# Kernel tuning notes

Measured on AMD Instinct MI355X. Metric: run time of the kernel, lower is better.

## Reference

```python
import jax, jax.numpy as jnp
import numpy as np

# Grid config: nuScenes-style BEV grid
XMIN, XMAX, DX = -51.2, 51.2, 0.4
YMIN, YMAX, DY = -51.2, 51.2, 0.4
ZMIN, ZMAX, DZ = -5.0, 3.0, 8.0
NX = int((XMAX - XMIN) / DX)  # 256
NY = int((YMAX - YMIN) / DY)  # 256
NZ = int((ZMAX - ZMIN) / DZ)  # 1
B, N, F = 8, 500000, 18       # batch, points per cloud, radar_feat_dim


def setup_inputs() -> dict:
    key = jax.random.key(0)
    pts = jax.random.normal(key, (B, N, F), dtype=jnp.float32)
    # spread xyz across the [-51.2, 51.2] grid (some points fall outside -> masked)
    pts = pts.at[..., :3].multiply(20.0)
    return {"points": pts}


def reference(points):
    """Scatter-mean rasterization of radar points into a dense BEV grid.

    points: (B, N, 18) float32. Returns (B, F*NZ, NY, NX).
    Equivalent math to the torch running-mean scatter: per-voxel mean of the
    18-dim features of all in-range points falling into that voxel.
    """
    x, y, z = points[..., 0], points[..., 1], points[..., 2]
    mask = ((x >= XMIN) & (x <= XMAX) &
            (y >= YMIN) & (y <= YMAX) &
            (z >= ZMIN) & (z <= ZMAX))
    sx, sy, sz = NX / (XMAX - XMIN), NY / (YMAX - YMIN), NZ / (ZMAX - ZMIN)
    ix = jnp.clip(((x - XMIN) * sx).astype(jnp.int32), 0, NX - 1)
    iy = jnp.clip(((y - YMIN) * sy).astype(jnp.int32), 0, NY - 1)
    iz = jnp.clip(((z - ZMIN) * sz).astype(jnp.int32), 0, NZ - 1)
    # global linear voxel index, batch-offset so one segment_sum covers all B
    lin = (iz * (NY * NX) + iy * NX + ix
           + jnp.arange(B, dtype=jnp.int32)[:, None] * (NZ * NY * NX))
    lin = lin.reshape(-1)                              # (B*N,)
    w = mask.astype(points.dtype).reshape(-1)          # (B*N,) 0/1 weights
    feats = points.reshape(-1, F) * w[:, None]         # masked-out -> 0 contribution
    nseg = B * NZ * NY * NX
    sums = jax.ops.segment_sum(feats, lin, num_segments=nseg)  # (nseg, F)
    cnts = jax.ops.segment_sum(w, lin, num_segments=nseg)      # (nseg,)
    mean = sums / jnp.maximum(cnts, 1.0)[:, None]
    grid = mean.reshape(B, NZ, NY, NX, F)
    grid = jnp.transpose(grid, (0, 4, 1, 2, 3))        # (B, F, NZ, NY, NX)
    return grid.reshape(B, F * NZ, NY, NX)
```

## Files before the change

kernel.cpp:

```cpp
#include <hip/hip_runtime.h>


#define B_     8
#define NPTS   500000
#define F_     18
#define NX_    256
#define NY_    256
#define NVOX   (NX_ * NY_)
#define BN     (B_ * NPTS)
#define NVOXT  (B_ * NVOX)
#define CAP    32

__global__ __launch_bounds__(256) void bin_kernel(const float* __restrict__ pts,
                                                  unsigned* __restrict__ cnt,
                                                  unsigned* __restrict__ list) {
    __shared__ float sh[256 * F_];
    const int tid = threadIdx.x;

    const float2* __restrict__ gp =
        (const float2*)(pts + (size_t)blockIdx.x * (256 * F_));
    float2* sp = (float2*)sh;
#pragma unroll
    for (int k = 0; k < 9; ++k)
        sp[tid + 256 * k] = gp[tid + 256 * k];
    __syncthreads();

    float x = sh[tid * F_ + 0];
    float y = sh[tid * F_ + 1];
    float z = sh[tid * F_ + 2];
    bool ok = (x >= -51.2f) & (x <= 51.2f) &
              (y >= -51.2f) & (y <= 51.2f) &
              (z >= -5.0f)  & (z <= 3.0f);
    if (!ok) return;

    int p  = blockIdx.x * 256 + tid;
    int ix = min(max((int)((x + 51.2f) * 2.5f), 0), NX_ - 1);
    int iy = min(max((int)((y + 51.2f) * 2.5f), 0), NY_ - 1);
    int b  = p / NPTS;
    int vox = b * NVOX + iy * NX_ + ix;

    unsigned slot = atomicAdd(cnt + vox, 1u);
    if (slot < CAP) list[(size_t)slot * NVOXT + vox] = (unsigned)p;
}

__global__ __launch_bounds__(256) void reduce_kernel(const float* __restrict__ pts,
                                                     const unsigned* __restrict__ cnt,
                                                     const unsigned* __restrict__ list,
                                                     float* __restrict__ out) {
    int v = blockIdx.x * 256 + threadIdx.x;
    int b   = v >> 16;
    int pos = v & (NVOX - 1);

    unsigned c = min(cnt[v], (unsigned)CAP);

    float s[F_];
#pragma unroll
    for (int f = 0; f < F_; ++f) s[f] = 0.0f;

    for (unsigned i = 0; i < c; ++i) {
        unsigned p = list[(size_t)i * NVOXT + v];
        const float2* rp = (const float2*)(pts + (size_t)p * F_);
#pragma unroll
        for (int j = 0; j < 9; ++j) {
            float2 t = rp[j];
            s[2 * j]     += t.x;
            s[2 * j + 1] += t.y;
        }
    }

    float rcp = (c > 0) ? (1.0f / (float)c) : 0.0f;
    float* ob = out + (((size_t)b * F_) << 16) + pos;
#pragma unroll
    for (int f = 0; f < F_; ++f) ob[(size_t)f << 16] = s[f] * rcp;
}

extern "C" void kernel_launch(void* const* d_in, const int* in_sizes, int n_in,
                              void* d_out, int out_size, void* d_ws, size_t ws_size,
                              hipStream_t stream) {
    const float* pts = (const float*)d_in[0];
    float* out = (float*)d_out;
    unsigned* cnt  = (unsigned*)d_ws;
    unsigned* list = cnt + NVOXT;

    hipMemsetAsync(cnt, 0, (size_t)NVOXT * sizeof(unsigned), stream);

    bin_kernel<<<BN / 256, 256, 0, stream>>>(pts, cnt, list);
    reduce_kernel<<<NVOXT / 256, 256, 0, stream>>>(pts, cnt, list, out);
}
```

Baseline: 425.3 us.

## Replace bin-list gather with direct float atomic scatter-sum of features

Drops the two-phase scheme that recorded capped per-voxel point lists and then re-read points in a gather. Each in-range point now atomically adds its 18 features into a per-voxel sum buffer and increments a count, and a finalize kernel divides and transposes. This removes the scattered list writes and the gathered point re-reads, but adds 18 float atomics per point and a larger workspace memset. It also removes the 32-point cap, and float atomic ordering makes summation order nondeterministic.

Measured after the change: 922.0 us. +116.8%, slower.

```diff
diff --git a/kernel.cpp b/kernel.cpp
--- a/kernel.cpp
+++ b/kernel.cpp
@@ -9,11 +9,10 @@
 #define NVOX   (NX_ * NY_)
 #define BN     (B_ * NPTS)
 #define NVOXT  (B_ * NVOX)
-#define CAP    32
 
-__global__ __launch_bounds__(256) void bin_kernel(const float* __restrict__ pts,
-                                                  unsigned* __restrict__ cnt,
-                                                  unsigned* __restrict__ list) {
+__global__ __launch_bounds__(256) void scatter_kernel(const float* __restrict__ pts,
+                                                      float* __restrict__ sums,
+                                                      unsigned* __restrict__ cnt) {
     __shared__ float sh[256 * F_];
     const int tid = threadIdx.x;
 
@@ -39,36 +38,32 @@
     int b  = p / NPTS;
     int vox = b * NVOX + iy * NX_ + ix;
 
-    unsigned slot = atomicAdd(cnt + vox, 1u);
-    if (slot < CAP) list[(size_t)slot * NVOXT + vox] = (unsigned)p;
+    float* s = sums + (size_t)vox * F_;
+#pragma unroll
+    for (int f = 0; f < F_; ++f)
+        unsafeAtomicAdd(s + f, sh[tid * F_ + f]);
+    atomicAdd(cnt + vox, 1u);
 }
 
-__global__ __launch_bounds__(256) void reduce_kernel(const float* __restrict__ pts,
-                                                     const unsigned* __restrict__ cnt,
-                                                     const unsigned* __restrict__ list,
-                                                     float* __restrict__ out) {
+__global__ __launch_bounds__(256) void finalize_kernel(const float* __restrict__ sums,
+                                                       const unsigned* __restrict__ cnt,
+                                                       float* __restrict__ out) {
     int v = blockIdx.x * 256 + threadIdx.x;
     int b   = v >> 16;
     int pos = v & (NVOX - 1);
 
-    unsigned c = min(cnt[v], (unsigned)CAP);
+    unsigned c = cnt[v];
+    float rcp = (c > 0) ? (1.0f / (float)c) : 0.0f;
 
+    const float2* sp = (const float2*)(sums + (size_t)v * F_);
     float s[F_];
 #pragma unroll
-    for (int f = 0; f < F_; ++f) s[f] = 0.0f;
-
-    for (unsigned i = 0; i < c; ++i) {
-        unsigned p = list[(size_t)i * NVOXT + v];
-        const float2* rp = (const float2*)(pts + (size_t)p * F_);
-#pragma unroll
-        for (int j = 0; j < 9; ++j) {
-            float2 t = rp[j];
-            s[2 * j]     += t.x;
-            s[2 * j + 1] += t.y;
-        }
+    for (int j = 0; j < 9; ++j) {
+        float2 t = sp[j];
+        s[2 * j]     = t.x;
+        s[2 * j + 1] = t.y;
     }
 
-    float rcp = (c > 0) ? (1.0f / (float)c) : 0.0f;
     float* ob = out + (((size_t)b * F_) << 16) + pos;
 #pragma unroll
     for (int f = 0; f < F_; ++f) ob[(size_t)f << 16] = s[f] * rcp;
@@ -79,11 +74,11 @@
                               hipStream_t stream) {
     const float* pts = (const float*)d_in[0];
     float* out = (float*)d_out;
-    unsigned* cnt  = (unsigned*)d_ws;
-    unsigned* list = cnt + NVOXT;
+    float* sums    = (float*)d_ws;
+    unsigned* cnt  = (unsigned*)(sums + (size_t)NVOXT * F_);
 
-    hipMemsetAsync(cnt, 0, (size_t)NVOXT * sizeof(unsigned), stream);
+    hipMemsetAsync(d_ws, 0, (size_t)NVOXT * (F_ + 1) * sizeof(float), stream);
 
-    bin_kernel<<<BN / 256, 256, 0, stream>>>(pts, cnt, list);
-    reduce_kernel<<<NVOXT / 256, 256, 0, stream>>>(pts, cnt, list, out);
+    scatter_kernel<<<BN / 256, 256, 0, stream>>>(pts, sums, cnt);
+    finalize_kernel<<<NVOXT / 256, 256, 0, stream>>>(sums, cnt, out);
 }
```
